# Optimization experiments

Hardware: AMD Instinct MI355X
Metric: run time of the kernel (lower is better)

The kernel has to match this reference:

```python
import jax, jax.numpy as jnp
import numpy as np

N_NODES = 100000
N_EDGES = 3200000
INPUT_DIM = 128
HIDDEN = 64


def spmm(row, col, vals, x, n):
    # out[i] = sum_{e: row[e]==i} vals[e] * x[col[e]]  -- COO SpMM via gather + segment_sum
    msgs = vals[:, None] * x[col]  # [E, F]
    return jax.ops.segment_sum(msgs, row, num_segments=n)


def setup_inputs() -> dict:
    key = jax.random.key(0)
    ks = jax.random.split(key, 12)
    embeddings = jax.random.normal(ks[0], (N_NODES, INPUT_DIM), dtype=jnp.float32)
    norm_degrees = jax.random.uniform(ks[1], (N_NODES, 1), dtype=jnp.float32)
    seed_mask = (jax.random.uniform(ks[2], (N_NODES, 1)) < 0.05).astype(jnp.float32)
    adj_row = jax.random.randint(ks[3], (N_EDGES,), 0, N_NODES, dtype=jnp.int32)
    adj_col = jax.random.randint(ks[4], (N_EDGES,), 0, N_NODES, dtype=jnp.int32)
    adj_vals = jax.random.uniform(ks[5], (N_EDGES,), dtype=jnp.float32)
    d_in = INPUT_DIM + 2
    # Linear params (torch Linear: y = x @ W.T + b); store W as [in, out]
    W1 = jax.random.normal(ks[6], (d_in, HIDDEN), dtype=jnp.float32) / np.sqrt(d_in)
    b1 = jnp.zeros((HIDDEN,), dtype=jnp.float32)
    W2 = jax.random.normal(ks[7], (HIDDEN, HIDDEN), dtype=jnp.float32) / np.sqrt(HIDDEN)
    b2 = jnp.zeros((HIDDEN,), dtype=jnp.float32)
    W_out = jax.random.normal(ks[8], (HIDDEN, 1), dtype=jnp.float32) / np.sqrt(HIDDEN)
    b_out = jnp.zeros((1,), dtype=jnp.float32)
    return {
        "embeddings": embeddings, "norm_degrees": norm_degrees, "seed_mask": seed_mask,
        "adj_row": adj_row, "adj_col": adj_col, "adj_vals": adj_vals,
        "W1": W1, "b1": b1, "W2": W2, "b2": b2, "W_out": W_out, "b_out": b_out,
    }


def reference(embeddings, norm_degrees, seed_mask, adj_row, adj_col, adj_vals,
              W1, b1, W2, b2, W_out, b_out):
    n = embeddings.shape[0]
    x = jnp.concatenate([embeddings, norm_degrees, seed_mask], axis=1)  # [N, input_dim+2]
    x = x @ W1 + b1                       # conv1
    x = jax.nn.relu(spmm(adj_row, adj_col, adj_vals, x, n))
    x = x @ W2 + b2                       # conv2
    x = jax.nn.relu(spmm(adj_row, adj_col, adj_vals, x, n))
    graph_rep = jnp.sum(x, axis=0)        # [HIDDEN]
    return graph_rep @ W_out + b_out      # [1]
```

## Files before the change

### kernel.cpp

```cpp
#include <hip/hip_runtime.h>
#include <hip/hip_bf16.h>

#define HID 64
#define IN_EMB 128
#define IN_DIM 130
#define ROWS_PER_BKT 512
#define LOG_RPB 9
#define MAX_BKT 256
#define PART_CHUNK 4096
#define SLOT_E 18432
#define W1TS 160
#define RPB 32
#define ECAP 2048

typedef __hip_bfloat16 bf16;
typedef __attribute__((ext_vector_type(8))) short bf16x8;
typedef __attribute__((ext_vector_type(4))) float fx4;
typedef __attribute__((ext_vector_type(2))) float fx2;

__device__ __forceinline__ short f2bfs(float f) {
  __hip_bfloat16 h = __float2bfloat16(f);
  return *(reinterpret_cast<short*>(&h));
}
__device__ __forceinline__ int pk_fp8x4(float a, float b, float c, float d) {
  int v = __builtin_amdgcn_cvt_pk_fp8_f32(a, b, 0, false);
  v = __builtin_amdgcn_cvt_pk_fp8_f32(c, d, v, true);
  return v;
}
__device__ __forceinline__ unsigned char f2fp8(float x) {
  return (unsigned char)(__builtin_amdgcn_cvt_pk_fp8_f32(x, x, 0, false) & 0xFF);
}

__global__ __launch_bounds__(256) void wprep_kernel(
    const float* __restrict__ W1, const float* __restrict__ W2,
    short* __restrict__ w1t, short* __restrict__ w2t) {
  const int t = threadIdx.x;
  if (blockIdx.x == 0) {
    for (int idx = t; idx < 64 * W1TS; idx += 256) {
      int c = idx / W1TS, k = idx % W1TS;
      w1t[idx] = f2bfs((k < IN_DIM) ? W1[k * HID + c] : 0.f);
    }
  } else {
    for (int idx = t; idx < 64 * 64; idx += 256) {
      int c = idx >> 6, k = idx & 63;
      w2t[idx] = f2bfs(W2[k * HID + c]);
    }
  }
}

__global__ __launch_bounds__(1024) void bscan_kernel(const int* __restrict__ bcnt,
                                                     int* __restrict__ bstart,
                                                     int* __restrict__ row_ptr,
                                                     int n, int nbkt) {
  __shared__ int s[1024];
  const int t = threadIdx.x;
  const int v = (t < nbkt) ? bcnt[t] : 0;
  s[t] = v;
  __syncthreads();
  for (int off = 1; off < 1024; off <<= 1) {
    int u = (t >= off) ? s[t - off] : 0;
    __syncthreads();
    s[t] += u;
    __syncthreads();
  }
  if (t < nbkt) bstart[t] = s[t] - v;
  if (t == 0) { bstart[nbkt] = s[1023]; row_ptr[n] = s[1023]; }
}

__global__ __launch_bounds__(512) void partition_kernel(
    const int* __restrict__ row, const int* __restrict__ col,
    const float* __restrict__ vals, int* __restrict__ bcur,
    int2* __restrict__ tmp, int nE) {
  __shared__ int2 lbuf[PART_CHUNK];
  __shared__ unsigned char lbid[PART_CHUNK];
  __shared__ int h[MAX_BKT];
  __shared__ int sc[MAX_BKT];
  __shared__ int lofs[MAX_BKT + 1];
  __shared__ int lcur[MAX_BKT];
  __shared__ int gbase[MAX_BKT];
  const int t = threadIdx.x;
  const int base = blockIdx.x * PART_CHUNK;
  const int cntE = min(PART_CHUNK, nE - base);

  if (t < MAX_BKT) h[t] = 0;
  __syncthreads();
  for (int kk = t; kk < PART_CHUNK / 4; kk += 512) {
    int e0 = base + kk * 4;
    if (e0 + 3 < nE) {
      int4 r4 = ((const int4*)row)[(base >> 2) + kk];
      atomicAdd(&h[r4.x >> LOG_RPB], 1);
      atomicAdd(&h[r4.y >> LOG_RPB], 1);
      atomicAdd(&h[r4.z >> LOG_RPB], 1);
      atomicAdd(&h[r4.w >> LOG_RPB], 1);
    } else {
      for (int j = 0; j < 4; ++j) {
        int e = e0 + j;
        if (e < nE) atomicAdd(&h[row[e] >> LOG_RPB], 1);
      }
    }
  }
  __syncthreads();
  if (t < MAX_BKT) sc[t] = h[t];
  __syncthreads();
  for (int off = 1; off < MAX_BKT; off <<= 1) {
    int u = (t < MAX_BKT && t >= off) ? sc[t - off] : 0;
    __syncthreads();
    if (t < MAX_BKT) sc[t] += u;
    __syncthreads();
  }
  if (t < MAX_BKT) {
    int ex = sc[t] - h[t];
    lofs[t] = ex;
    lcur[t] = ex;
    if (h[t] > 0) gbase[t] = t * SLOT_E + atomicAdd(&bcur[t], h[t]);
  }
  if (t == MAX_BKT - 1) lofs[MAX_BKT] = sc[t];
  __syncthreads();
  for (int kk = t; kk < PART_CHUNK / 4; kk += 512) {
    int e0 = base + kk * 4;
    if (e0 + 3 < nE) {
      int4 r4 = ((const int4*)row)[(base >> 2) + kk];
      int4 c4 = ((const int4*)col)[(base >> 2) + kk];
      float4 v4 = ((const float4*)vals)[(base >> 2) + kk];
      int rr[4] = {r4.x, r4.y, r4.z, r4.w};
      int cc[4] = {c4.x, c4.y, c4.z, c4.w};
      float vv[4] = {v4.x, v4.y, v4.z, v4.w};
#pragma unroll
      for (int j = 0; j < 4; ++j) {
        int b = rr[j] >> LOG_RPB;
        int p = atomicAdd(&lcur[b], 1);
        lbuf[p] = make_int2(cc[j] | ((rr[j] & (ROWS_PER_BKT - 1)) << 20),
                            __float_as_int(vv[j]));
        lbid[p] = (unsigned char)b;
      }
    } else {
      for (int j = 0; j < 4; ++j) {
        int e = e0 + j;
        if (e < nE) {
          int r = row[e];
          int b = r >> LOG_RPB;
          int p = atomicAdd(&lcur[b], 1);
          lbuf[p] = make_int2(col[e] | ((r & (ROWS_PER_BKT - 1)) << 20),
                              __float_as_int(vals[e]));
          lbid[p] = (unsigned char)b;
        }
      }
    }
  }
  __syncthreads();
  for (int i = t; i < cntE; i += 512) {
    int b = lbid[i];
    int off = i - lofs[b];
    int g = gbase[b] + off;
    if (g - b * SLOT_E < SLOT_E) tmp[g] = lbuf[i];
  }
}

__global__ __launch_bounds__(512) void bucket_sort_kernel(
    const int* __restrict__ bstart, const int2* __restrict__ tmp,
    int2* __restrict__ ce, int* __restrict__ row_ptr, int n) {
  __shared__ int rcnt[ROWS_PER_BKT];
  __shared__ int rpos[ROWS_PER_BKT];
  __shared__ int sc[ROWS_PER_BKT];
  const int t = threadIdx.x;
  const int b = blockIdx.x;
  const int start = bstart[b];
  const int len   = bstart[b + 1] - start;
  const int2* ts = tmp + (size_t)b * SLOT_E;
  rcnt[t] = 0;
  __syncthreads();
  const int* keys = (const int*)ts;
  for (int i = t; i < len; i += 512)
    atomicAdd(&rcnt[((unsigned)keys[2 * i]) >> 20], 1);
  __syncthreads();
  sc[t] = rcnt[t];
  __syncthreads();
  for (int off = 1; off < ROWS_PER_BKT; off <<= 1) {
    int u = (t >= off) ? sc[t - off] : 0;
    __syncthreads();
    sc[t] += u;
    __syncthreads();
  }
  {
    int ex = sc[t] - rcnt[t];
    int gpos = start + ex;
    rpos[t] = gpos;
    int gr = b * ROWS_PER_BKT + t;
    if (gr < n) row_ptr[gr] = gpos;
  }
  __syncthreads();
  for (int i = t; i < len; i += 512) {
    int2 e = ts[i];
    int p = atomicAdd(&rpos[((unsigned)e.x) >> 20], 1);
    ce[p] = make_int2(e.x & 0xFFFFF, e.y);
  }
}

__global__ __launch_bounds__(256) void lin1_kernel(
    const float* __restrict__ emb, const float* __restrict__ deg,
    const float* __restrict__ seed, const short* __restrict__ w1t,
    const float* __restrict__ b1, unsigned char* __restrict__ out, int n) {
  const int t = threadIdx.x;
  const int base = blockIdx.x * 64;
  const int lane = t & 63, w = t >> 6;
  const int nl = lane & 15, q = lane >> 4;
  const short* pB = w1t + nl * W1TS + q * 8;
  const float bias0 = b1[nl], bias1 = b1[16 + nl],
              bias2 = b1[32 + nl], bias3 = b1[48 + nl];

  const int anode = base + w * 16 + nl;
  bf16x8 afr[5];
  if (anode < n) {
    const float4* ep = (const float4*)(emb + (size_t)anode * IN_EMB);
#pragma unroll
    for (int kt = 0; kt < 4; ++kt) {
      float4 v0 = ep[q * 2 + kt * 8];
      float4 v1 = ep[q * 2 + 1 + kt * 8];
      bf16x8 a;
      a[0] = f2bfs(v0.x); a[1] = f2bfs(v0.y); a[2] = f2bfs(v0.z); a[3] = f2bfs(v0.w);
      a[4] = f2bfs(v1.x); a[5] = f2bfs(v1.y); a[6] = f2bfs(v1.z); a[7] = f2bfs(v1.w);
      afr[kt] = a;
    }
    bf16x8 a4 = {0, 0, 0, 0, 0, 0, 0, 0};
    if (q == 0) { a4[0] = f2bfs(deg[anode]); a4[1] = f2bfs(seed[anode]); }
    afr[4] = a4;
  } else {
#pragma unroll
    for (int kt = 0; kt < 5; ++kt) afr[kt] = (bf16x8){0, 0, 0, 0, 0, 0, 0, 0};
  }

  fx4 ac0 = {0.f, 0.f, 0.f, 0.f}, ac1 = ac0, ac2 = ac0, ac3 = ac0;
#pragma unroll
  for (int kt = 0; kt < 5; ++kt) {
    bf16x8 b0  = *(const bf16x8*)(pB + kt * 32);
    bf16x8 b1v = *(const bf16x8*)(pB + 16 * W1TS + kt * 32);
    bf16x8 b2v = *(const bf16x8*)(pB + 32 * W1TS + kt * 32);
    bf16x8 b3v = *(const bf16x8*)(pB + 48 * W1TS + kt * 32);
    ac0 = __builtin_amdgcn_mfma_f32_16x16x32_bf16(afr[kt], b0,  ac0, 0, 0, 0);
    ac1 = __builtin_amdgcn_mfma_f32_16x16x32_bf16(afr[kt], b1v, ac1, 0, 0, 0);
    ac2 = __builtin_amdgcn_mfma_f32_16x16x32_bf16(afr[kt], b2v, ac2, 0, 0, 0);
    ac3 = __builtin_amdgcn_mfma_f32_16x16x32_bf16(afr[kt], b3v, ac3, 0, 0, 0);
  }
#pragma unroll
  for (int r = 0; r < 4; ++r) {
    int node = base + w * 16 + q * 4 + r;
    if (node < n) {
      unsigned char* o = out + ((size_t)node << 6);
      o[nl]      = f2fp8(ac0[r] + bias0);
      o[16 + nl] = f2fp8(ac1[r] + bias1);
      o[32 + nl] = f2fp8(ac2[r] + bias2);
      o[48 + nl] = f2fp8(ac3[r] + bias3);
    }
  }
}

#define GLD(ev, u)                                                            \
  const uint2 u = *(const uint2*)(xp + (((size_t)(unsigned)(ev)) << 6) + 8 * fl);
#define GMAD(ev, u)                                                           \
  {                                                                           \
    const float v = __int_as_float((int)((ev) >> 32));                        \
    const fx2 v2 = {v, v};                                                    \
    a0 += v2 * __builtin_amdgcn_cvt_pk_f32_fp8(u.x, false);                   \
    a1 += v2 * __builtin_amdgcn_cvt_pk_f32_fp8(u.x, true);                    \
    a2 += v2 * __builtin_amdgcn_cvt_pk_f32_fp8(u.y, false);                   \
    a3 += v2 * __builtin_amdgcn_cvt_pk_f32_fp8(u.y, true);                    \
  }
#define GMAD_P(ev, u, ok)                                                     \
  {                                                                           \
    const float v = (ok) ? __int_as_float((int)((ev) >> 32)) : 0.f;           \
    const fx2 v2 = {v, v};                                                    \
    a0 += v2 * __builtin_amdgcn_cvt_pk_f32_fp8(u.x, false);                   \
    a1 += v2 * __builtin_amdgcn_cvt_pk_f32_fp8(u.x, true);                    \
    a2 += v2 * __builtin_amdgcn_cvt_pk_f32_fp8(u.y, false);                   \
    a3 += v2 * __builtin_amdgcn_cvt_pk_f32_fp8(u.y, true);                    \
  }

#define SPMM_STAGE_EDGES                                                      \
  const unsigned long long* cep = (const unsigned long long*)ce;              \
  const int r0blk = blockIdx.x * RPB;                                         \
  const int bstartE = row_ptr[r0blk];                                         \
  const int bendE = row_ptr[(r0blk + RPB < n) ? (r0blk + RPB) : n];           \
  const int cnt = min(bendE - bstartE, ECAP);                                 \
  for (int ii = threadIdx.x; ii < cnt; ii += 256)                             \
    eb[ii] = __builtin_nontemporal_load(cep + bstartE + ii);                  \
  __syncthreads();

#define SPMM_GATHER_BODY                                                      \
  const int i0r = row_ptr[r];                                                 \
  const int endr = row_ptr[r + 1];                                            \
  const int lend = endr - bstartE;                                            \
  if (lend <= cnt) {                                                          \
    int i = i0r - bstartE;                                                    \
    for (; i + 4 <= lend; i += 4) {                                           \
      unsigned long long e0 = eb[i];                                          \
      unsigned long long e1 = eb[i + 1];                                      \
      unsigned long long e2 = eb[i + 2];                                      \
      unsigned long long e3 = eb[i + 3];                                      \
      GLD(e0, u0); GLD(e1, u1); GLD(e2, u2); GLD(e3, u3);                     \
      GMAD(e0, u0); GMAD(e1, u1); GMAD(e2, u2); GMAD(e3, u3);                 \
    }                                                                         \
    if (i < lend) {                                                           \
      const int last = lend - 1;                                              \
      bool k1 = i + 1 < lend, k2 = i + 2 < lend, k3 = i + 3 < lend;           \
      unsigned long long e0 = eb[i];                                          \
      unsigned long long e1 = eb[k1 ? i + 1 : last];                          \
      unsigned long long e2 = eb[k2 ? i + 2 : last];                          \
      unsigned long long e3 = eb[k3 ? i + 3 : last];                          \
      GLD(e0, u0); GLD(e1, u1); GLD(e2, u2); GLD(e3, u3);                     \
      GMAD(e0, u0); GMAD_P(e1, u1, k1);                                       \
      GMAD_P(e2, u2, k2); GMAD_P(e3, u3, k3);                                 \
    }                                                                         \
  } else {                                                                    \
    int i = i0r;                                                              \
    for (; i + 4 <= endr; i += 4) {                                           \
      unsigned long long e0 = __builtin_nontemporal_load(cep + i);            \
      unsigned long long e1 = __builtin_nontemporal_load(cep + i + 1);        \
      unsigned long long e2 = __builtin_nontemporal_load(cep + i + 2);        \
      unsigned long long e3 = __builtin_nontemporal_load(cep + i + 3);        \
      GLD(e0, u0); GLD(e1, u1); GLD(e2, u2); GLD(e3, u3);                     \
      GMAD(e0, u0); GMAD(e1, u1); GMAD(e2, u2); GMAD(e3, u3);                 \
    }                                                                         \
    if (i < endr) {                                                           \
      const int last = endr - 1;                                              \
      bool k1 = i + 1 < endr, k2 = i + 2 < endr, k3 = i + 3 < endr;           \
      unsigned long long e0 = cep[i];                                         \
      unsigned long long e1 = cep[k1 ? i + 1 : last];                         \
      unsigned long long e2 = cep[k2 ? i + 2 : last];                         \
      unsigned long long e3 = cep[k3 ? i + 3 : last];                         \
      GLD(e0, u0); GLD(e1, u1); GLD(e2, u2); GLD(e3, u3);                     \
      GMAD(e0, u0); GMAD_P(e1, u1, k1);                                       \
      GMAD_P(e2, u2, k2); GMAD_P(e3, u3, k3);                                 \
    }                                                                         \
  }

__global__ __launch_bounds__(256) void spmm_csr_kernel(
    const int* __restrict__ row_ptr, const int2* __restrict__ ce,
    const unsigned char* __restrict__ x, unsigned char* __restrict__ y, int n) {
  __shared__ unsigned long long eb[ECAP];
  const int fl = threadIdx.x & 7;
  const int r = blockIdx.x * RPB + (threadIdx.x >> 3);
  const unsigned char* xp = x;
  SPMM_STAGE_EDGES
  if (r < n) {
    fx2 a0 = {0.f, 0.f}, a1 = a0, a2 = a0, a3 = a0;
    SPMM_GATHER_BODY
    int lo = pk_fp8x4(fmaxf(a0.x, 0.f), fmaxf(a0.y, 0.f),
                      fmaxf(a1.x, 0.f), fmaxf(a1.y, 0.f));
    int hi = pk_fp8x4(fmaxf(a2.x, 0.f), fmaxf(a2.y, 0.f),
                      fmaxf(a3.x, 0.f), fmaxf(a3.y, 0.f));
    *(int2*)(y + ((size_t)r << 6) + 8 * fl) = make_int2(lo, hi);
  }
}

__global__ __launch_bounds__(256) void lin2_kernel(
    const unsigned char* __restrict__ yin, const short* __restrict__ w2t,
    const float* __restrict__ b2, unsigned char* __restrict__ xout, int n) {
  const int t = threadIdx.x;
  const int base = blockIdx.x * 64;
  const int lane = t & 63, w = t >> 6;
  const int nl = lane & 15, q = lane >> 4;
  const short* pB = w2t + nl * 64 + q * 8;
  const float bias0 = b2[nl], bias1 = b2[16 + nl],
              bias2 = b2[32 + nl], bias3 = b2[48 + nl];

  const int anode = base + w * 16 + nl;
  const unsigned char* xg = yin + (((size_t)anode) << 6) + q * 8;
  fx4 ac0 = {0.f, 0.f, 0.f, 0.f}, ac1 = ac0, ac2 = ac0, ac3 = ac0;
#pragma unroll
  for (int kt = 0; kt < 2; ++kt) {
    uint2 u8 = (anode < n) ? *(const uint2*)(xg + kt * 32) : make_uint2(0u, 0u);
    fx2 f0 = __builtin_amdgcn_cvt_pk_f32_fp8(u8.x, false);
    fx2 f1 = __builtin_amdgcn_cvt_pk_f32_fp8(u8.x, true);
    fx2 f2 = __builtin_amdgcn_cvt_pk_f32_fp8(u8.y, false);
    fx2 f3 = __builtin_amdgcn_cvt_pk_f32_fp8(u8.y, true);
    bf16x8 a;
    a[0] = f2bfs(f0.x); a[1] = f2bfs(f0.y); a[2] = f2bfs(f1.x); a[3] = f2bfs(f1.y);
    a[4] = f2bfs(f2.x); a[5] = f2bfs(f2.y); a[6] = f2bfs(f3.x); a[7] = f2bfs(f3.y);
    bf16x8 b0  = *(const bf16x8*)(pB + kt * 32);
    bf16x8 b1v = *(const bf16x8*)(pB + 16 * 64 + kt * 32);
    bf16x8 b2v = *(const bf16x8*)(pB + 32 * 64 + kt * 32);
    bf16x8 b3v = *(const bf16x8*)(pB + 48 * 64 + kt * 32);
    ac0 = __builtin_amdgcn_mfma_f32_16x16x32_bf16(a, b0,  ac0, 0, 0, 0);
    ac1 = __builtin_amdgcn_mfma_f32_16x16x32_bf16(a, b1v, ac1, 0, 0, 0);
    ac2 = __builtin_amdgcn_mfma_f32_16x16x32_bf16(a, b2v, ac2, 0, 0, 0);
    ac3 = __builtin_amdgcn_mfma_f32_16x16x32_bf16(a, b3v, ac3, 0, 0, 0);
  }
#pragma unroll
  for (int r = 0; r < 4; ++r) {
    int node = base + w * 16 + q * 4 + r;
    if (node < n) {
      unsigned char* o = xout + ((size_t)node << 6);
      o[nl]      = f2fp8(ac0[r] + bias0);
      o[16 + nl] = f2fp8(ac1[r] + bias1);
      o[32 + nl] = f2fp8(ac2[r] + bias2);
      o[48 + nl] = f2fp8(ac3[r] + bias3);
    }
  }
}

__global__ __launch_bounds__(256) void spmm2_fused_kernel(
    const int* __restrict__ row_ptr, const int2* __restrict__ ce,
    const unsigned char* __restrict__ x, const float* __restrict__ Wout,
    float* __restrict__ partials, int n) {
  __shared__ unsigned long long eb[ECAP];
  const int fl = threadIdx.x & 7;
  const int r = blockIdx.x * RPB + (threadIdx.x >> 3);
  const unsigned char* xp = x;
  SPMM_STAGE_EDGES
  float wpart = 0.f;
  if (r < n) {
    fx2 a0 = {0.f, 0.f}, a1 = a0, a2 = a0, a3 = a0;
    SPMM_GATHER_BODY
    const float4 wv0 = ((const float4*)Wout)[2 * fl];
    const float4 wv1 = ((const float4*)Wout)[2 * fl + 1];
    wpart = fmaxf(a0.x, 0.f) * wv0.x + fmaxf(a0.y, 0.f) * wv0.y
          + fmaxf(a1.x, 0.f) * wv0.z + fmaxf(a1.y, 0.f) * wv0.w
          + fmaxf(a2.x, 0.f) * wv1.x + fmaxf(a2.y, 0.f) * wv1.y
          + fmaxf(a3.x, 0.f) * wv1.z + fmaxf(a3.y, 0.f) * wv1.w;
  }
  for (int off = 32; off; off >>= 1) wpart += __shfl_down(wpart, off, 64);
  __shared__ float part[4];
  const int lane = threadIdx.x & 63;
  if (lane == 0) part[threadIdx.x >> 6] = wpart;
  __syncthreads();
  if (threadIdx.x == 0)
    partials[blockIdx.x] = part[0] + part[1] + part[2] + part[3];
}

__global__ __launch_bounds__(1024) void reduce_kernel(
    const float* __restrict__ partials, const float* __restrict__ bout,
    float* __restrict__ out, int m) {
  const int t = threadIdx.x;
  float s = 0.f;
  const int m4 = m >> 2;
  for (int i = t; i < m4; i += 1024) {
    float4 v = ((const float4*)partials)[i];
    s += v.x + v.y + v.z + v.w;
  }
  if (t < (m & 3)) s += partials[(m & ~3) + t];
  for (int off = 32; off; off >>= 1) s += __shfl_down(s, off, 64);
  __shared__ float wsum[16];
  if ((t & 63) == 0) wsum[t >> 6] = s;
  __syncthreads();
  if (t == 0) {
    float tot = bout[0];
    for (int w = 0; w < 16; ++w) tot += wsum[w];
    out[0] = tot;
  }
}

extern "C" void kernel_launch(void* const* d_in, const int* in_sizes, int n_in,
                              void* d_out, int out_size, void* d_ws, size_t ws_size,
                              hipStream_t stream) {
  const float* emb  = (const float*)d_in[0];
  const float* deg  = (const float*)d_in[1];
  const float* seed = (const float*)d_in[2];
  const int*   row  = (const int*)d_in[3];
  const int*   col  = (const int*)d_in[4];
  const float* vals = (const float*)d_in[5];
  const float* W1   = (const float*)d_in[6];
  const float* b1   = (const float*)d_in[7];
  const float* W2   = (const float*)d_in[8];
  const float* b2   = (const float*)d_in[9];
  const float* Wout = (const float*)d_in[10];
  const float* bout = (const float*)d_in[11];
  float* out = (float*)d_out;

  const int n  = in_sizes[0] / IN_EMB;
  const int nE = in_sizes[3];
  const int nbkt = (n + ROWS_PER_BKT - 1) / ROWS_PER_BKT;

  const int lin_blocks  = (n + 63) / 64;
  const int row_blocks  = (n + RPB - 1) / RPB;
  const int part_blocks = (nE + PART_CHUNK - 1) / PART_CHUNK;

  char* ws = (char*)d_ws;
  int2* ce   = (int2*)ws;  ws += (size_t)nE * sizeof(int2);
  char* tmpb = ws;
  int2* tmp  = (int2*)ws;  ws += (size_t)nbkt * SLOT_E * sizeof(int2);
  unsigned char* xb = (unsigned char*)ws;  ws += ((size_t)n * HID + 255) & ~255ULL;
  int* row_ptr = (int*)ws; ws += ((size_t)(n + 1) * 4 + 255) & ~255ULL;
  int* bcur    = (int*)ws; ws += ((size_t)nbkt * 4 + 255) & ~255ULL;
  int* bstart  = (int*)ws; ws += ((size_t)(nbkt + 1) * 4 + 255) & ~255ULL;
  short* w1t   = (short*)ws; ws += ((size_t)64 * W1TS * 2 + 255) & ~255ULL;
  short* w2t   = (short*)ws; ws += ((size_t)64 * 64 * 2 + 255) & ~255ULL;
  float* partials = (float*)ws;
  unsigned char* xa = (unsigned char*)tmpb;
  unsigned char* ya = (unsigned char*)(tmpb + (8u << 20));

  hipMemsetAsync(bcur, 0, (size_t)nbkt * sizeof(int), stream);
  wprep_kernel<<<2, 256, 0, stream>>>(W1, W2, w1t, w2t);
  partition_kernel<<<part_blocks, 512, 0, stream>>>(row, col, vals, bcur, tmp, nE);
  bscan_kernel<<<1, 1024, 0, stream>>>(bcur, bstart, row_ptr, n, nbkt);
  bucket_sort_kernel<<<nbkt, 512, 0, stream>>>(bstart, tmp, ce, row_ptr, n);

  lin1_kernel<<<lin_blocks, 256, 0, stream>>>(emb, deg, seed, w1t, b1, xa, n);
  spmm_csr_kernel<<<row_blocks, 256, 0, stream>>>(row_ptr, ce, xa, ya, n);
  lin2_kernel<<<lin_blocks, 256, 0, stream>>>(ya, w2t, b2, xb, n);
  spmm2_fused_kernel<<<row_blocks, 256, 0, stream>>>(row_ptr, ce, xb, Wout, partials, n);
  reduce_kernel<<<1, 1024, 0, stream>>>(partials, bout, out, row_blocks);
}
```

Baseline: 292.5 us.

## Drop memset and bucket-scan launches; stage lin1/lin2 inputs through LDS

The hipMemsetAsync that zeroed bucket counters moves into an extra block of wprep_kernel. The separate single-block scan kernel is removed, and every bucket_sort block recomputes the 256-entry prefix sum locally, which cuts two launches from the serial chain. lin1 and lin2 now load their input tiles into padded shared memory with coalesced loads before the MFMA loop, instead of each lane reading strided rows from global memory. The trade-off is redundant scan work in each bucket-sort block and added LDS use plus a barrier in the linear kernels.

```diff
diff --git a/kernel.cpp b/kernel.cpp
--- a/kernel.cpp
+++ b/kernel.cpp
@@ -10,6 +10,8 @@
 #define PART_CHUNK 4096
 #define SLOT_E 18432
 #define W1TS 160
+#define SASTR 168
+#define SYSTR 72
 #define RPB 32
 #define ECAP 2048
 
@@ -33,38 +35,21 @@
 
 __global__ __launch_bounds__(256) void wprep_kernel(
     const float* __restrict__ W1, const float* __restrict__ W2,
-    short* __restrict__ w1t, short* __restrict__ w2t) {
+    short* __restrict__ w1t, short* __restrict__ w2t, int* __restrict__ bcur) {
   const int t = threadIdx.x;
   if (blockIdx.x == 0) {
     for (int idx = t; idx < 64 * W1TS; idx += 256) {
       int c = idx / W1TS, k = idx % W1TS;
       w1t[idx] = f2bfs((k < IN_DIM) ? W1[k * HID + c] : 0.f);
     }
-  } else {
+  } else if (blockIdx.x == 1) {
     for (int idx = t; idx < 64 * 64; idx += 256) {
       int c = idx >> 6, k = idx & 63;
       w2t[idx] = f2bfs(W2[k * HID + c]);
     }
-  }
-}
-
-__global__ __launch_bounds__(1024) void bscan_kernel(const int* __restrict__ bcnt,
-                                                     int* __restrict__ bstart,
-                                                     int* __restrict__ row_ptr,
-                                                     int n, int nbkt) {
-  __shared__ int s[1024];
-  const int t = threadIdx.x;
-  const int v = (t < nbkt) ? bcnt[t] : 0;
-  s[t] = v;
-  __syncthreads();
-  for (int off = 1; off < 1024; off <<= 1) {
-    int u = (t >= off) ? s[t - off] : 0;
-    __syncthreads();
-    s[t] += u;
-    __syncthreads();
-  }
-  if (t < nbkt) bstart[t] = s[t] - v;
-  if (t == 0) { bstart[nbkt] = s[1023]; row_ptr[n] = s[1023]; }
+  } else {
+    if (t < MAX_BKT) bcur[t] = 0;
+  }
 }
 
 __global__ __launch_bounds__(512) void partition_kernel(
@@ -157,15 +142,26 @@
 }
 
 __global__ __launch_bounds__(512) void bucket_sort_kernel(
-    const int* __restrict__ bstart, const int2* __restrict__ tmp,
+    const int* __restrict__ bcurf, const int2* __restrict__ tmp,
     int2* __restrict__ ce, int* __restrict__ row_ptr, int n) {
+  __shared__ int binc[MAX_BKT];
+  __shared__ int bcnt_s[MAX_BKT];
   __shared__ int rcnt[ROWS_PER_BKT];
   __shared__ int rpos[ROWS_PER_BKT];
   __shared__ int sc[ROWS_PER_BKT];
   const int t = threadIdx.x;
   const int b = blockIdx.x;
-  const int start = bstart[b];
-  const int len   = bstart[b + 1] - start;
+  if (t < MAX_BKT) { int c = bcurf[t]; bcnt_s[t] = c; binc[t] = c; }
+  __syncthreads();
+  for (int off = 1; off < MAX_BKT; off <<= 1) {
+    int u = (t < MAX_BKT && t >= off) ? binc[t - off] : 0;
+    __syncthreads();
+    if (t < MAX_BKT) binc[t] += u;
+    __syncthreads();
+  }
+  const int start = binc[b] - bcnt_s[b];
+  const int len   = bcnt_s[b];
+  if (b == gridDim.x - 1 && t == 0) row_ptr[n] = binc[MAX_BKT - 1];
   const int2* ts = tmp + (size_t)b * SLOT_E;
   rcnt[t] = 0;
   __syncthreads();
@@ -200,46 +196,53 @@
     const float* __restrict__ emb, const float* __restrict__ deg,
     const float* __restrict__ seed, const short* __restrict__ w1t,
     const float* __restrict__ b1, unsigned char* __restrict__ out, int n) {
+  __shared__ short sA[64 * SASTR];
   const int t = threadIdx.x;
   const int base = blockIdx.x * 64;
+
+  for (int idx = t; idx < 64 * 32; idx += 256) {
+    int nn = idx >> 5, k4 = idx & 31;
+    int node = base + nn;
+    short4 wv;
+    if (node < n) {
+      float4 v = ((const float4*)emb)[(size_t)node * 32 + k4];
+      wv = make_short4(f2bfs(v.x), f2bfs(v.y), f2bfs(v.z), f2bfs(v.w));
+    } else {
+      wv = make_short4(0, 0, 0, 0);
+    }
+    *(short4*)&sA[nn * SASTR + 4 * k4] = wv;
+  }
+  for (int idx = t; idx < 64 * 32; idx += 256) {
+    int nn = idx >> 5, kk = idx & 31;
+    int node = base + nn;
+    float v = 0.f;
+    if (node < n) {
+      if (kk == 0) v = deg[node];
+      else if (kk == 1) v = seed[node];
+    }
+    sA[nn * SASTR + 128 + kk] = f2bfs(v);
+  }
+  __syncthreads();
+
   const int lane = t & 63, w = t >> 6;
   const int nl = lane & 15, q = lane >> 4;
+  const short* pA = &sA[(w * 16 + nl) * SASTR + q * 8];
   const short* pB = w1t + nl * W1TS + q * 8;
   const float bias0 = b1[nl], bias1 = b1[16 + nl],
               bias2 = b1[32 + nl], bias3 = b1[48 + nl];
 
-  const int anode = base + w * 16 + nl;
-  bf16x8 afr[5];
-  if (anode < n) {
-    const float4* ep = (const float4*)(emb + (size_t)anode * IN_EMB);
-#pragma unroll
-    for (int kt = 0; kt < 4; ++kt) {
-      float4 v0 = ep[q * 2 + kt * 8];
-      float4 v1 = ep[q * 2 + 1 + kt * 8];
-      bf16x8 a;
-      a[0] = f2bfs(v0.x); a[1] = f2bfs(v0.y); a[2] = f2bfs(v0.z); a[3] = f2bfs(v0.w);
-      a[4] = f2bfs(v1.x); a[5] = f2bfs(v1.y); a[6] = f2bfs(v1.z); a[7] = f2bfs(v1.w);
-      afr[kt] = a;
-    }
-    bf16x8 a4 = {0, 0, 0, 0, 0, 0, 0, 0};
-    if (q == 0) { a4[0] = f2bfs(deg[anode]); a4[1] = f2bfs(seed[anode]); }
-    afr[4] = a4;
-  } else {
-#pragma unroll
-    for (int kt = 0; kt < 5; ++kt) afr[kt] = (bf16x8){0, 0, 0, 0, 0, 0, 0, 0};
-  }
-
   fx4 ac0 = {0.f, 0.f, 0.f, 0.f}, ac1 = ac0, ac2 = ac0, ac3 = ac0;
 #pragma unroll
   for (int kt = 0; kt < 5; ++kt) {
+    bf16x8 a   = *(const bf16x8*)(pA + kt * 32);
     bf16x8 b0  = *(const bf16x8*)(pB + kt * 32);
     bf16x8 b1v = *(const bf16x8*)(pB + 16 * W1TS + kt * 32);
     bf16x8 b2v = *(const bf16x8*)(pB + 32 * W1TS + kt * 32);
     bf16x8 b3v = *(const bf16x8*)(pB + 48 * W1TS + kt * 32);
-    ac0 = __builtin_amdgcn_mfma_f32_16x16x32_bf16(afr[kt], b0,  ac0, 0, 0, 0);
-    ac1 = __builtin_amdgcn_mfma_f32_16x16x32_bf16(afr[kt], b1v, ac1, 0, 0, 0);
-    ac2 = __builtin_amdgcn_mfma_f32_16x16x32_bf16(afr[kt], b2v, ac2, 0, 0, 0);
-    ac3 = __builtin_amdgcn_mfma_f32_16x16x32_bf16(afr[kt], b3v, ac3, 0, 0, 0);
+    ac0 = __builtin_amdgcn_mfma_f32_16x16x32_bf16(a, b0,  ac0, 0, 0, 0);
+    ac1 = __builtin_amdgcn_mfma_f32_16x16x32_bf16(a, b1v, ac1, 0, 0, 0);
+    ac2 = __builtin_amdgcn_mfma_f32_16x16x32_bf16(a, b2v, ac2, 0, 0, 0);
+    ac3 = __builtin_amdgcn_mfma_f32_16x16x32_bf16(a, b3v, ac3, 0, 0, 0);
   }
 #pragma unroll
   for (int r = 0; r < 4; ++r) {
@@ -355,20 +358,29 @@
 __global__ __launch_bounds__(256) void lin2_kernel(
     const unsigned char* __restrict__ yin, const short* __restrict__ w2t,
     const float* __restrict__ b2, unsigned char* __restrict__ xout, int n) {
+  __shared__ unsigned char sY[64 * SYSTR];
   const int t = threadIdx.x;
   const int base = blockIdx.x * 64;
+  {
+    int nn = t >> 2, c4 = t & 3;
+    int node = base + nn;
+    uint4 v = make_uint4(0u, 0u, 0u, 0u);
+    if (node < n) v = ((const uint4*)yin)[(size_t)node * 4 + c4];
+    *(uint4*)&sY[nn * SYSTR + 16 * c4] = v;
+  }
+  __syncthreads();
+
   const int lane = t & 63, w = t >> 6;
   const int nl = lane & 15, q = lane >> 4;
+  const unsigned char* pY = &sY[(w * 16 + nl) * SYSTR + q * 8];
   const short* pB = w2t + nl * 64 + q * 8;
   const float bias0 = b2[nl], bias1 = b2[16 + nl],
               bias2 = b2[32 + nl], bias3 = b2[48 + nl];
 
-  const int anode = base + w * 16 + nl;
-  const unsigned char* xg = yin + (((size_t)anode) << 6) + q * 8;
   fx4 ac0 = {0.f, 0.f, 0.f, 0.f}, ac1 = ac0, ac2 = ac0, ac3 = ac0;
 #pragma unroll
   for (int kt = 0; kt < 2; ++kt) {
-    uint2 u8 = (anode < n) ? *(const uint2*)(xg + kt * 32) : make_uint2(0u, 0u);
+    uint2 u8 = *(const uint2*)(pY + kt * 32);
     fx2 f0 = __builtin_amdgcn_cvt_pk_f32_fp8(u8.x, false);
     fx2 f1 = __builtin_amdgcn_cvt_pk_f32_fp8(u8.x, true);
     fx2 f2 = __builtin_amdgcn_cvt_pk_f32_fp8(u8.y, false);
@@ -480,19 +492,16 @@
   int2* tmp  = (int2*)ws;  ws += (size_t)nbkt * SLOT_E * sizeof(int2);
   unsigned char* xb = (unsigned char*)ws;  ws += ((size_t)n * HID + 255) & ~255ULL;
   int* row_ptr = (int*)ws; ws += ((size_t)(n + 1) * 4 + 255) & ~255ULL;
-  int* bcur    = (int*)ws; ws += ((size_t)nbkt * 4 + 255) & ~255ULL;
-  int* bstart  = (int*)ws; ws += ((size_t)(nbkt + 1) * 4 + 255) & ~255ULL;
+  int* bcur    = (int*)ws; ws += ((size_t)MAX_BKT * 4 + 255) & ~255ULL;
   short* w1t   = (short*)ws; ws += ((size_t)64 * W1TS * 2 + 255) & ~255ULL;
   short* w2t   = (short*)ws; ws += ((size_t)64 * 64 * 2 + 255) & ~255ULL;
   float* partials = (float*)ws;
   unsigned char* xa = (unsigned char*)tmpb;
   unsigned char* ya = (unsigned char*)(tmpb + (8u << 20));
 
-  hipMemsetAsync(bcur, 0, (size_t)nbkt * sizeof(int), stream);
-  wprep_kernel<<<2, 256, 0, stream>>>(W1, W2, w1t, w2t);
+  wprep_kernel<<<3, 256, 0, stream>>>(W1, W2, w1t, w2t, bcur);
   partition_kernel<<<part_blocks, 512, 0, stream>>>(row, col, vals, bcur, tmp, nE);
-  bscan_kernel<<<1, 1024, 0, stream>>>(bcur, bstart, row_ptr, n, nbkt);
-  bucket_sort_kernel<<<nbkt, 512, 0, stream>>>(bstart, tmp, ce, row_ptr, n);
+  bucket_sort_kernel<<<nbkt, 512, 0, stream>>>(bcur, tmp, ce, row_ptr, n);
 
   lin1_kernel<<<lin_blocks, 256, 0, stream>>>(emb, deg, seed, w1t, b1, xa, n);
   spmm_csr_kernel<<<row_blocks, 256, 0, stream>>>(row_ptr, ce, xa, ya, n);
```

After: 291.4 us. No clear change (-0.4%).
